# Performance work log

Hardware: AMD Instinct MI355X
Metric: run time of the kernel (lower is better)

The kernel has to match this reference:

```python
import jax, jax.numpy as jnp
import numpy as np
import math

D_MODEL = 1024
NUM_HEADS = 16
HEAD_DIM = D_MODEL // NUM_HEADS
THETA = 10000.0
B, S = 2, 2048


def _rope(x, positions, theta):
    # x: (b, h, s, d); positions: (s,) int
    d = x.shape[-1]
    inv_freq = theta ** (-jnp.arange(0, d, 2, dtype=jnp.float32) / d)  # (d/2,)
    ang = positions.astype(jnp.float32)[:, None] * inv_freq[None, :]   # (s, d/2)
    cos, sin = jnp.cos(ang), jnp.sin(ang)
    x1 = x[..., ::2]
    x2 = x[..., 1::2]
    r1 = x1 * cos - x2 * sin
    r2 = x1 * sin + x2 * cos
    # interleave back to (..., d)
    return jnp.stack([r1, r2], axis=-1).reshape(x.shape)


def setup_inputs() -> dict:
    key = jax.random.key(0)
    ks = jax.random.split(key, 5)
    std = math.sqrt(2.0 / (D_MODEL + D_MODEL))
    return {
        "x": jax.random.normal(ks[0], (B, S, D_MODEL), dtype=jnp.float32),
        "token_positions": jnp.arange(S, dtype=jnp.int32),
        "Wq": jax.random.normal(ks[1], (D_MODEL, D_MODEL), dtype=jnp.float32) * std,
        "Wk": jax.random.normal(ks[2], (D_MODEL, D_MODEL), dtype=jnp.float32) * std,
        "Wv": jax.random.normal(ks[3], (D_MODEL, D_MODEL), dtype=jnp.float32) * std,
        "Wo": jax.random.normal(ks[4], (D_MODEL, D_MODEL), dtype=jnp.float32) * std,
    }


def reference(x, token_positions, Wq, Wk, Wv, Wo):
    b, s, _ = x.shape
    def split_heads(t):
        return t.reshape(b, s, NUM_HEADS, HEAD_DIM).transpose(0, 2, 1, 3)  # (b,h,s,d)
    Q = split_heads(x @ Wq.T)
    K = split_heads(x @ Wk.T)
    V = split_heads(x @ Wv.T)
    Q = _rope(Q, token_positions, THETA)
    K = _rope(K, token_positions, THETA)
    scores = jnp.einsum("bhqd,bhkd->bhqk", Q, K) / math.sqrt(HEAD_DIM)
    causal = jnp.tril(jnp.ones((s, s), dtype=bool))
    scores = jnp.where(causal, scores, -jnp.inf)
    attn = jax.nn.softmax(scores, axis=-1)
    out = jnp.einsum("bhqk,bhkd->bhqd", attn, V)
    out = out.transpose(0, 2, 1, 3).reshape(b, s, D_MODEL)
    return out @ Wo.T
```

## Files before the change

kernel.cpp:

```cpp
#include <hip/hip_runtime.h>
#include <math.h>

typedef unsigned short u16;
typedef unsigned int   u32;
typedef __attribute__((ext_vector_type(8))) short bf16x8;
typedef __attribute__((ext_vector_type(4))) float floatx4;
typedef __attribute__((ext_vector_type(4))) _Float16 halfx4;
typedef __attribute__((ext_vector_type(2))) unsigned int uintx2;

#define SEQ 2048
#define DM  1024
#define NH  16
#define DH  64
#define MM  4096
#define QSCALE 0.18033688011112042f

__device__ __forceinline__ u16 f2bf(float f) {
    u32 u = __builtin_bit_cast(u32, f);
    u += 0x7fffu + ((u >> 16) & 1u);
    return (u16)(u >> 16);
}

__device__ __forceinline__ void async16(const void* g, void* l) {
    __builtin_amdgcn_global_load_lds(
        (const __attribute__((address_space(1))) void*)g,
        (__attribute__((address_space(3))) void*)l, 16, 0, 0);
}

__global__ __launch_bounds__(256) void prep_kernel(const float* __restrict__ x,
                                                   const float* __restrict__ w0,
                                                   const float* __restrict__ w1,
                                                   const float* __restrict__ w2,
                                                   const float* __restrict__ w3,
                                                   u16* __restrict__ Xsh,
                                                   u16* __restrict__ Wsh,
                                                   const int* __restrict__ pos,
                                                   float2* __restrict__ tab) {
    const int bid = blockIdx.x, cb = blockIdx.y, tid = threadIdx.x;

    int lin = bid * 16 + cb;
    if (lin < 256) {
        int i = lin * 256 + tid;
        int p = i >> 5, d2 = i & 31;
        float freq = __expf(-(float)d2 * (9.2103403719761836f / 32.0f));
        float sv, cv;
        sincosf((float)pos[p] * freq, &sv, &cv);
        tab[i] = make_float2(cv, sv);
    }

    const float* src; u16* dst; int row0;
    if (bid < 64) { src = x; dst = Xsh; row0 = bid * 64; }
    else {
        int wi = (bid - 64) >> 4;
        src = (wi == 0) ? w0 : (wi == 1) ? w1 : (wi == 2) ? w2 : w3;
        dst = Wsh + (size_t)wi * DM * DM;
        row0 = ((bid - 64) & 15) * 64;
    }
    __shared__ __align__(16) u16 t[64 * 64];
#pragma unroll
    for (int rep = 0; rep < 4; ++rep) {
        int f = rep * 256 + tid;
        int r = f >> 4, c4 = f & 15;
        float4 v = *(const float4*)&src[(size_t)(row0 + r) * DM + cb * 64 + c4 * 4];
        uint2 pk;
        pk.x = (u32)f2bf(v.x) | ((u32)f2bf(v.y) << 16);
        pk.y = (u32)f2bf(v.z) | ((u32)f2bf(v.w) << 16);
        int ch = (c4 >> 1) ^ (r & 7);
        *(uint2*)&t[r * 64 + ch * 8 + (c4 & 1) * 4] = pk;
    }
    __syncthreads();
#pragma unroll
    for (int rep = 0; rep < 2; ++rep) {
        int s = rep * 256 + tid;
        int tile = s >> 6, l = s & 63;
        int mt = tile >> 1, kt = tile & 1, lm = l & 15, quad = l >> 4;
        int m = mt * 16 + lm;
        uint4 v = *(const uint4*)&t[m * 64 + ((kt * 4 + quad) ^ (m & 7)) * 8];
        size_t rowblk = (size_t)(row0 >> 4) + mt;
        size_t ktile  = cb * 2 + kt;
        *(uint4*)&dst[(rowblk * 32 + ktile) * 512 + l * 8] = v;
    }
}

template<int NZ, bool OUTF32>
__global__ __launch_bounds__(256, 2) void gemm_f(const u16* __restrict__ Ash,
                                                 const u16* __restrict__ Wbase,
                                                 u16* __restrict__ outbf,
                                                 float* __restrict__ outf,
                                                 _Float16* __restrict__ vtout,
                                                 const float2* __restrict__ ropetab) {
    const int m0 = blockIdx.x * 64, n0 = blockIdx.y * 128;
    const int tid = threadIdx.x, lane = tid & 63, w = tid >> 6;
    const int lm = lane & 15, quad = lane >> 4;
    const int rb0 = m0 >> 4;
    const int cb0 = n0 >> 4;

    __shared__ __align__(16) u16 lsA[2][4 * 512];
    __shared__ __align__(16) u16 lsB[2][NZ * 8 * 512];

    const u16* aSrc = Ash + ((size_t)(rb0 + w) * 32) * 512 + lane * 8;
    constexpr int NPW = NZ * 2;
    const u16* bSrc[NPW];
#pragma unroll
    for (int j = 0; j < NPW; ++j) {
        int p = w * NPW + j, z = p >> 3, cb8 = p & 7;
        bSrc[j] = Wbase + (size_t)z * (DM * DM)
                + ((size_t)(cb0 + cb8) * 32) * 512 + lane * 8;
    }

    auto stage = [&](int buf, int it) {
        async16(aSrc + (size_t)it * 512, &lsA[buf][w * 512 + lane * 8]);
#pragma unroll
        for (int j = 0; j < NPW; ++j)
            async16(bSrc[j] + (size_t)it * 512,
                    &lsB[buf][(w * NPW + j) * 512 + lane * 8]);
    };

    floatx4 acc[NZ][4][2];
    const floatx4 z4 = {0.f, 0.f, 0.f, 0.f};
#pragma unroll
    for (int z = 0; z < NZ; ++z)
#pragma unroll
        for (int mt = 0; mt < 4; ++mt)
#pragma unroll
            for (int nt = 0; nt < 2; ++nt) acc[z][mt][nt] = z4;

    stage(0, 0);
    __syncthreads();

#pragma unroll 2
    for (int it = 0; it < 32; ++it) {
        if (it < 31) stage((it + 1) & 1, it + 1);
        const u16* La = &lsA[it & 1][0];
        const u16* Lb = &lsB[it & 1][0];
        bf16x8 a[4], b[NZ][2];
#pragma unroll
        for (int mt = 0; mt < 4; ++mt)
            a[mt] = *(const bf16x8*)&La[mt * 512 + lane * 8];
#pragma unroll
        for (int z = 0; z < NZ; ++z)
#pragma unroll
            for (int nt = 0; nt < 2; ++nt)
                b[z][nt] = *(const bf16x8*)&Lb[(z * 8 + w * 2 + nt) * 512 + lane * 8];
#pragma unroll
        for (int z = 0; z < NZ; ++z)
#pragma unroll
            for (int mt = 0; mt < 4; ++mt)
#pragma unroll
                for (int nt = 0; nt < 2; ++nt)
                    acc[z][mt][nt] = __builtin_amdgcn_mfma_f32_16x16x32_bf16(
                        a[mt], b[z][nt], acc[z][mt][nt], 0, 0, 0);
        __syncthreads();
    }

#pragma unroll
    for (int z = 0; z < NZ; ++z) {
        if (!OUTF32 && NZ == 3 && z == 2) {
#pragma unroll
            for (int mt = 0; mt < 4; ++mt) {
                int row = m0 + mt * 16;
                int b = row >> 11;
                int sblk = (row & (SEQ - 1)) >> 4;
#pragma unroll
                for (int nt = 0; nt < 2; ++nt) {
                    int col = n0 + w * 32 + nt * 16;
                    int h = col >> 6;
                    int dblk = (col & 63) >> 4;
                    size_t chunk = ((size_t)(b * NH + h) * 128 + sblk) * 4 + dblk;
                    uint2 pk;
                    pk.x = __builtin_bit_cast(u32, __builtin_amdgcn_cvt_pkrtz(acc[z][mt][nt][0], acc[z][mt][nt][1]));
                    pk.y = __builtin_bit_cast(u32, __builtin_amdgcn_cvt_pkrtz(acc[z][mt][nt][2], acc[z][mt][nt][3]));
                    *(uint2*)&vtout[chunk * 256 + lane * 4] = pk;
                }
            }
            continue;
        }
        const bool rope = !OUTF32;
        const float osc = (!OUTF32 && z == 0) ? QSCALE : 1.0f;
#pragma unroll
        for (int mt = 0; mt < 4; ++mt)
#pragma unroll
            for (int r = 0; r < 4; ++r) {
                int row = m0 + mt * 16 + quad * 4 + r;
#pragma unroll
                for (int nt = 0; nt < 2; ++nt) {
                    int col = n0 + w * 32 + nt * 16 + lm;
                    float v  = acc[z][mt][nt][r];
                    if (rope) {
                        float pv = __shfl_xor(v, 1);
                        float2 cs = ropetab[(row & (SEQ - 1)) * 32 + ((col & 63) >> 1)];
                        v = (lm & 1) ? fmaf(pv, cs.y, v * cs.x) : fmaf(v, cs.x, -pv * cs.y);
                    }
                    v *= osc;
                    if (OUTF32) {
                        outf[(size_t)row * DM + col] = v;
                    } else {
                        float hv = __shfl_xor(v, 1);
                        if (!(lm & 1)) {
                            u32 pk = (u32)f2bf(v) | ((u32)f2bf(hv) << 16);
                            *(u32*)&outbf[(size_t)z * ((size_t)MM * DM) + (size_t)row * DM + col] = pk;
                        }
                    }
                }
            }
    }
}

__global__ __launch_bounds__(256, 4) void attn_kernel(const u16* __restrict__ Q,
                                                      const u16* __restrict__ K,
                                                      const _Float16* __restrict__ Vf,
                                                      u16* __restrict__ AO) {
    const int u  = blockIdx.x;
    const int qt = (u < 256) ? (15 - (u >> 5)) : ((u >> 5) - 8);
    const int bh = u & 31;
    const int b  = bh >> 4, h = bh & 15;
    const int q0 = qt * 128;
    const int tid = threadIdx.x, w = tid >> 6, lane = tid & 63;
    const int lm = lane & 15, quad = lane >> 4;

    __shared__ __align__(16) u16      lsK[2][8 * 512];
    __shared__ __align__(16) _Float16 lsV[2][16 * 256];

    bf16x8 qb[2][2];
#pragma unroll
    for (int qi = 0; qi < 2; ++qi)
#pragma unroll
        for (int ks = 0; ks < 2; ++ks)
            qb[qi][ks] = *(const bf16x8*)
                &Q[(size_t)(b * SEQ + q0 + w * 32 + qi * 16 + lm) * DM + h * DH + ks * 32 + quad * 8];

    const floatx4 z4 = {0.f, 0.f, 0.f, 0.f};
    floatx4 o[2][4];
    floatx4 o5[2];
#pragma unroll
    for (int qi = 0; qi < 2; ++qi) {
#pragma unroll
        for (int dt = 0; dt < 4; ++dt) o[qi][dt] = z4;
        o5[qi] = z4;
    }

    const u16* Kb = K + (size_t)(b * SEQ) * DM + h * DH + (size_t)lm * DM + quad * 8;
    const _Float16* Vb = Vf + (size_t)bh * (128 * 4 * 256);

    auto stageKV = [&](int buf, int kt) {
#pragma unroll
        for (int j = 0; j < 2; ++j) {
            int c = w * 2 + j;
            async16(Kb + (size_t)(kt * 64 + (c >> 1) * 16) * DM + (c & 1) * 32,
                    &lsK[buf][c * 512 + lane * 8]);
        }
#pragma unroll
        for (int p = 0; p < 2; ++p) {
            int off = p * 2048 + w * 512 + lane * 8;
            async16(Vb + (size_t)kt * 4096 + off, &lsV[buf][off]);
        }
    };

    stageKV(0, 0);
    const int nkt = 2 * qt + 2;
    const halfx4 ones = {(_Float16)1.f, (_Float16)1.f, (_Float16)1.f, (_Float16)1.f};

    for (int kt = 0; kt < nkt; ++kt) {
        __syncthreads();
        if (kt + 1 < nkt) stageKV((kt + 1) & 1, kt + 1);
        const u16*      Lk = lsK[kt & 1];
        const _Float16* Lv = lsV[kt & 1];

        floatx4 s4[2][4];
#pragma unroll
        for (int qi = 0; qi < 2; ++qi)
#pragma unroll
            for (int st = 0; st < 4; ++st) s4[qi][st] = z4;
#pragma unroll
        for (int ks = 0; ks < 2; ++ks)
#pragma unroll
            for (int st = 0; st < 4; ++st) {
                bf16x8 ka = *(const bf16x8*)&Lk[(st * 2 + ks) * 512 + lane * 8];
#pragma unroll
                for (int qi = 0; qi < 2; ++qi)
                    s4[qi][st] = __builtin_amdgcn_mfma_f32_16x16x32_bf16(ka, qb[qi][ks], s4[qi][st], 0, 0, 0);
            }

        const int rel = kt - 2 * qt;
#pragma unroll
        for (int st = 0; st < 4; ++st) {
            halfx4 pb2[2];
#pragma unroll
            for (int qi = 0; qi < 2; ++qi) {
#pragma unroll
                for (int r = 0; r < 4; ++r) {
                    float v = s4[qi][st][r];
                    if (rel >= 0) {
                        int keyloc = rel * 64 + st * 16 + quad * 4 + r;
                        if (keyloc > w * 32 + qi * 16 + lm) v = -1e30f;
                    }
                    s4[qi][st][r] = exp2f(v);
                }
                uintx2 pk2;
                pk2.x = __builtin_bit_cast(u32, __builtin_amdgcn_cvt_pkrtz(s4[qi][st][0], s4[qi][st][1]));
                pk2.y = __builtin_bit_cast(u32, __builtin_amdgcn_cvt_pkrtz(s4[qi][st][2], s4[qi][st][3]));
                pb2[qi] = __builtin_bit_cast(halfx4, pk2);
            }
#pragma unroll
            for (int dt = 0; dt < 4; ++dt) {
                halfx4 va = *(const halfx4*)&Lv[(st * 4 + dt) * 256 + lane * 4];
#pragma unroll
                for (int qi = 0; qi < 2; ++qi)
                    o[qi][dt] = __builtin_amdgcn_mfma_f32_16x16x16f16(va, pb2[qi], o[qi][dt], 0, 0, 0);
            }
#pragma unroll
            for (int qi = 0; qi < 2; ++qi)
                o5[qi] = __builtin_amdgcn_mfma_f32_16x16x16f16(ones, pb2[qi], o5[qi], 0, 0, 0);
        }
    }

    float rl[2] = {1.0f / o5[0][0], 1.0f / o5[1][0]};

    __syncthreads();
    u16* eb = (u16*)&lsK[0][0];
#pragma unroll
    for (int qi = 0; qi < 2; ++qi) {
        const int q = w * 32 + qi * 16 + lm;
#pragma unroll
        for (int dt = 0; dt < 4; ++dt) {
            uint2 pk;
            pk.x = (u32)f2bf(o[qi][dt][0] * rl[qi]) | ((u32)f2bf(o[qi][dt][1] * rl[qi]) << 16);
            pk.y = (u32)f2bf(o[qi][dt][2] * rl[qi]) | ((u32)f2bf(o[qi][dt][3] * rl[qi]) << 16);
            int ch = (dt * 2 + (quad >> 1)) ^ (lm & 7);
            *(uint2*)&eb[q * 64 + ch * 8 + (quad & 1) * 4] = pk;
        }
    }
    __syncthreads();
    const size_t rowblk0 = (size_t)((b * SEQ + q0) >> 4);
#pragma unroll
    for (int rbi = 0; rbi < 2; ++rbi) {
#pragma unroll
        for (int kt = 0; kt < 2; ++kt) {
            uint4 v = *(const uint4*)&eb[((w * 2 + rbi) * 16 + lm) * 64 + ((kt * 4 + quad) ^ (lm & 7)) * 8];
            *(uint4*)&AO[((rowblk0 + w * 2 + rbi) * 32 + (h * 2 + kt)) * 512 + lane * 8] = v;
        }
    }
}

extern "C" void kernel_launch(void* const* d_in, const int* in_sizes, int n_in,
                              void* d_out, int out_size, void* d_ws, size_t ws_size,
                              hipStream_t stream) {
    const float* x   = (const float*)d_in[0];
    const int*   pos = (const int*)d_in[1];
    float* out = (float*)d_out;

    u16* ws = (u16*)d_ws;
    const size_t MD = (size_t)MM * DM;
    const size_t DD = (size_t)DM * DM;
    u16* Xsh = ws;
    u16* Wsh = ws + MD;
    u16* Qbf = ws + MD + 4 * DD;
    u16* Kbf = Qbf + MD;
    u16* VtB = Kbf + MD;
    float2* ropetab = (float2*)(VtB + MD);
    _Float16* Vt = (_Float16*)VtB;
    u16* AOsh = Xsh;

    prep_kernel<<<dim3(128, 16), 256, 0, stream>>>(
        x, (const float*)d_in[2], (const float*)d_in[3], (const float*)d_in[4],
        (const float*)d_in[5], Xsh, Wsh, pos, ropetab);

    gemm_f<3, false><<<dim3(64, 8), 256, 0, stream>>>(
        Xsh, Wsh, Qbf, nullptr, Vt, ropetab);

    attn_kernel<<<dim3(512), 256, 0, stream>>>(Qbf, Kbf, Vt, AOsh);

    gemm_f<1, true><<<dim3(64, 8), 256, 0, stream>>>(
        AOsh, Wsh + 3 * DD, nullptr, out, nullptr, ropetab);
}
```

Before: 207.0 us.

## Write K in MFMA fragment layout and use 128-key attention tiles

The QKV GEMM epilogue now applies RoPE to K, stages it through LDS, and writes it in a pre-tiled per-head fragment layout. Attention can then load K with contiguous 16-byte async copies instead of strided row gathers. The attention loop now covers 128 keys per iteration with doubled K/V LDS buffers, which halves the iteration and barrier count. In exchange, LDS use and register pressure go up, and launch bounds drop from 4 to 2 blocks per SM, so occupancy falls. The diagonal tile also masks a larger wasted region.

```diff
diff --git a/kernel.cpp b/kernel.cpp
--- a/kernel.cpp
+++ b/kernel.cpp
@@ -88,6 +88,7 @@
                                                  u16* __restrict__ outbf,
                                                  float* __restrict__ outf,
                                                  _Float16* __restrict__ vtout,
+                                                 u16* __restrict__ koutbf,
                                                  const float2* __restrict__ ropetab) {
     const int m0 = blockIdx.x * 64, n0 = blockIdx.y * 128;
     const int tid = threadIdx.x, lane = tid & 63, w = tid >> 6;
@@ -171,6 +172,39 @@
                     pk.x = __builtin_bit_cast(u32, __builtin_amdgcn_cvt_pkrtz(acc[z][mt][nt][0], acc[z][mt][nt][1]));
                     pk.y = __builtin_bit_cast(u32, __builtin_amdgcn_cvt_pkrtz(acc[z][mt][nt][2], acc[z][mt][nt][3]));
                     *(uint2*)&vtout[chunk * 256 + lane * 4] = pk;
+                }
+            }
+            continue;
+        }
+        if (!OUTF32 && NZ == 3 && z == 1) {
+            u16* t = (u16*)&lsB[0][0];
+#pragma unroll
+            for (int mt = 0; mt < 4; ++mt)
+#pragma unroll
+                for (int r = 0; r < 4; ++r) {
+                    int row = m0 + mt * 16 + quad * 4 + r;
+#pragma unroll
+                    for (int nt = 0; nt < 2; ++nt) {
+                        int col = n0 + w * 32 + nt * 16 + lm;
+                        float v  = acc[z][mt][nt][r];
+                        float pv = __shfl_xor(v, 1);
+                        float2 cs = ropetab[(row & (SEQ - 1)) * 32 + ((col & 63) >> 1)];
+                        v = (lm & 1) ? fmaf(pv, cs.y, v * cs.x) : fmaf(v, cs.x, -pv * cs.y);
+                        t[(mt * 16 + quad * 4 + r) * 136 + (w * 32 + nt * 16 + lm)] = f2bf(v);
+                    }
+                }
+            __syncthreads();
+            {
+                int bb = m0 >> 11;
+                int sblk0 = (m0 & (SEQ - 1)) >> 4;
+                int h0 = n0 >> 6;
+#pragma unroll
+                for (int j = 0; j < 4; ++j) {
+                    int c = w * 4 + j;
+                    int hloc = c >> 3, sblkl = (c >> 1) & 3, ks2 = c & 1;
+                    uint4 v = *(const uint4*)&t[(sblkl * 16 + lm) * 136 + hloc * 64 + ks2 * 32 + quad * 8];
+                    size_t chunk = ((size_t)(bb * NH + h0 + hloc) * 128 + sblk0 + sblkl) * 2 + ks2;
+                    *(uint4*)&koutbf[chunk * 512 + lane * 8] = v;
                 }
             }
             continue;
@@ -206,8 +240,8 @@
     }
 }
 
-__global__ __launch_bounds__(256, 4) void attn_kernel(const u16* __restrict__ Q,
-                                                      const u16* __restrict__ K,
+__global__ __launch_bounds__(256, 2) void attn_kernel(const u16* __restrict__ Q,
+                                                      const u16* __restrict__ Kf,
                                                       const _Float16* __restrict__ Vf,
                                                       u16* __restrict__ AO) {
     const int u  = blockIdx.x;
@@ -218,8 +252,8 @@
     const int tid = threadIdx.x, w = tid >> 6, lane = tid & 63;
     const int lm = lane & 15, quad = lane >> 4;
 
-    __shared__ __align__(16) u16      lsK[2][8 * 512];
-    __shared__ __align__(16) _Float16 lsV[2][16 * 256];
+    __shared__ __align__(16) u16      lsK[2][16 * 512];
+    __shared__ __align__(16) _Float16 lsV[2][32 * 256];
 
     bf16x8 qb[2][2];
 #pragma unroll
@@ -239,59 +273,55 @@
         o5[qi] = z4;
     }
 
-    const u16* Kb = K + (size_t)(b * SEQ) * DM + h * DH + (size_t)lm * DM + quad * 8;
+    const u16*      Kb = Kf + (size_t)bh * (256 * 512);
     const _Float16* Vb = Vf + (size_t)bh * (128 * 4 * 256);
 
     auto stageKV = [&](int buf, int kt) {
 #pragma unroll
-        for (int j = 0; j < 2; ++j) {
-            int c = w * 2 + j;
-            async16(Kb + (size_t)(kt * 64 + (c >> 1) * 16) * DM + (c & 1) * 32,
-                    &lsK[buf][c * 512 + lane * 8]);
-        }
-#pragma unroll
-        for (int p = 0; p < 2; ++p) {
-            int off = p * 2048 + w * 512 + lane * 8;
-            async16(Vb + (size_t)kt * 4096 + off, &lsV[buf][off]);
+        for (int j = 0; j < 4; ++j) {
+            int kc = w * 4 + j;
+            async16(Kb + ((size_t)kt * 16 + kc) * 512 + lane * 8,
+                    &lsK[buf][kc * 512 + lane * 8]);
+            int off = w * 2048 + j * 512 + lane * 8;
+            async16(Vb + (size_t)kt * 8192 + off, &lsV[buf][off]);
         }
     };
 
     stageKV(0, 0);
-    const int nkt = 2 * qt + 2;
     const halfx4 ones = {(_Float16)1.f, (_Float16)1.f, (_Float16)1.f, (_Float16)1.f};
 
-    for (int kt = 0; kt < nkt; ++kt) {
+    for (int kt = 0; kt <= qt; ++kt) {
         __syncthreads();
-        if (kt + 1 < nkt) stageKV((kt + 1) & 1, kt + 1);
+        if (kt < qt) stageKV((kt + 1) & 1, kt + 1);
         const u16*      Lk = lsK[kt & 1];
         const _Float16* Lv = lsV[kt & 1];
 
-        floatx4 s4[2][4];
+        floatx4 s4[2][8];
 #pragma unroll
         for (int qi = 0; qi < 2; ++qi)
 #pragma unroll
-            for (int st = 0; st < 4; ++st) s4[qi][st] = z4;
+            for (int st = 0; st < 8; ++st) s4[qi][st] = z4;
 #pragma unroll
         for (int ks = 0; ks < 2; ++ks)
 #pragma unroll
-            for (int st = 0; st < 4; ++st) {
+            for (int st = 0; st < 8; ++st) {
                 bf16x8 ka = *(const bf16x8*)&Lk[(st * 2 + ks) * 512 + lane * 8];
 #pragma unroll
                 for (int qi = 0; qi < 2; ++qi)
                     s4[qi][st] = __builtin_amdgcn_mfma_f32_16x16x32_bf16(ka, qb[qi][ks], s4[qi][st], 0, 0, 0);
             }
 
-        const int rel = kt - 2 * qt;
-#pragma unroll
-        for (int st = 0; st < 4; ++st) {
+        const bool diag = (kt == qt);
+#pragma unroll
+        for (int st = 0; st < 8; ++st) {
             halfx4 pb2[2];
 #pragma unroll
             for (int qi = 0; qi < 2; ++qi) {
 #pragma unroll
                 for (int r = 0; r < 4; ++r) {
                     float v = s4[qi][st][r];
-                    if (rel >= 0) {
-                        int keyloc = rel * 64 + st * 16 + quad * 4 + r;
+                    if (diag) {
+                        int keyloc = st * 16 + quad * 4 + r;
                         if (keyloc > w * 32 + qi * 16 + lm) v = -1e30f;
                     }
                     s4[qi][st][r] = exp2f(v);
@@ -355,8 +385,8 @@
     u16* Xsh = ws;
     u16* Wsh = ws + MD;
     u16* Qbf = ws + MD + 4 * DD;
-    u16* Kbf = Qbf + MD;
-    u16* VtB = Kbf + MD;
+    u16* Kfb = Qbf + MD;
+    u16* VtB = Kfb + MD;
     float2* ropetab = (float2*)(VtB + MD);
     _Float16* Vt = (_Float16*)VtB;
     u16* AOsh = Xsh;
@@ -366,10 +396,10 @@
         (const float*)d_in[5], Xsh, Wsh, pos, ropetab);
 
     gemm_f<3, false><<<dim3(64, 8), 256, 0, stream>>>(
-        Xsh, Wsh, Qbf, nullptr, Vt, ropetab);
-
-    attn_kernel<<<dim3(512), 256, 0, stream>>>(Qbf, Kbf, Vt, AOsh);
+        Xsh, Wsh, Qbf, nullptr, Vt, Kfb, ropetab);
+
+    attn_kernel<<<dim3(512), 256, 0, stream>>>(Qbf, Kfb, Vt, AOsh);
 
     gemm_f<1, true><<<dim3(64, 8), 256, 0, stream>>>(
-        AOsh, Wsh + 3 * DD, nullptr, out, nullptr, ropetab);
-}
+        AOsh, Wsh + 3 * DD, nullptr, out, nullptr, nullptr, ropetab);
+}
```

Result: faster. 185.9 us (-10.2%).
